# Performance work log

Measured on AMD Instinct MI355X. Metric: run time of the kernel, lower is better.

## Reference

```python
import jax, jax.numpy as jnp
import numpy as np

N_NODES = 50000
N_EDGES = 1600000
N_DECODE = 500000
D = 128
EPS = 1e-6


def _sage_conv(x, src, dst, Wl, bl, Wr, n_nodes):
    # PyG SAGEConv (mean aggr): out = lin_l(mean_{j in N(i)} x_j) + lin_r(x_i)
    msg = x[src]                                            # [E, D] gather
    s = jax.ops.segment_sum(msg, dst, num_segments=n_nodes) # [N, D]
    cnt = jax.ops.segment_sum(jnp.ones((src.shape[0],), x.dtype), dst,
                              num_segments=n_nodes)         # [N]
    aggr = s / jnp.maximum(cnt, 1.0)[:, None]
    return aggr @ Wl + bl + x @ Wr


def setup_inputs() -> dict:
    key = jax.random.key(0)
    ks = jax.random.split(key, 9)
    scale = 1.0 / np.sqrt(D)
    x = jax.random.normal(ks[0], (N_NODES, D), dtype=jnp.float32)
    edge_index = jax.random.randint(ks[1], (2, N_EDGES), 0, N_NODES, dtype=jnp.int64)
    decode_index = jax.random.randint(ks[2], (2, N_DECODE), 0, N_NODES, dtype=jnp.int64)
    W1l = jax.random.normal(ks[3], (D, D), dtype=jnp.float32) * scale
    b1 = jnp.zeros((D,), dtype=jnp.float32)
    W1r = jax.random.normal(ks[4], (D, D), dtype=jnp.float32) * scale
    W2l = jax.random.normal(ks[5], (D, D), dtype=jnp.float32) * scale
    b2 = jnp.zeros((D,), dtype=jnp.float32)
    W2r = jax.random.normal(ks[6], (D, D), dtype=jnp.float32) * scale
    return {"x": x, "edge_index": edge_index, "decode_index": decode_index,
            "W1l": W1l, "b1": b1, "W1r": W1r, "W2l": W2l, "b2": b2, "W2r": W2r}


def reference(x, edge_index, decode_index, W1l, b1, W1r, W2l, b2, W2r):
    src, dst = edge_index[0], edge_index[1]
    h = _sage_conv(x, src, dst, W1l, b1, W1r, N_NODES)
    h = jax.nn.relu(h)
    # dropout is a no-op in eval mode (training=False)
    h = _sage_conv(h, src, dst, W2l, b2, W2r, N_NODES)
    a = h[decode_index[0]]                                  # [Dk, D]
    b = h[decode_index[1]]
    num = jnp.sum(a * b, axis=1)
    denom = jnp.maximum(jnp.linalg.norm(a, axis=1) * jnp.linalg.norm(b, axis=1), EPS)
    return jax.nn.sigmoid(num / denom)
```

## Files before the change

### kernel.cpp

```cpp
#include <hip/hip_runtime.h>
#include <cstddef>

#define D 128
#define NBITS 7
#define BCAP2 6144
#define CHUNK 4096
#define BSTRIDE8 36

typedef float floatx4 __attribute__((ext_vector_type(4)));
typedef float floatx2 __attribute__((ext_vector_type(2)));

__device__ __forceinline__ int incl_scan64(int v) {
    const int lane = threadIdx.x & 63;
#pragma unroll
    for (int o = 1; o < 64; o <<= 1) {
        int u = __shfl_up(v, o);
        if (lane >= o) v += u;
    }
    return v;
}

__device__ __forceinline__ void accf8p(floatx2* a2, uint4 u) {
    unsigned w[4] = {u.x, u.y, u.z, u.w};
#pragma unroll
    for (int k = 0; k < 4; ++k) {
        a2[2 * k + 0] += __builtin_amdgcn_cvt_pk_f32_fp8((int)w[k], false);
        a2[2 * k + 1] += __builtin_amdgcn_cvt_pk_f32_fp8((int)w[k], true);
    }
}

__device__ __forceinline__ float dotf8(uint4 ua, uint4 ub) {
    unsigned wa[4] = {ua.x, ua.y, ua.z, ua.w};
    unsigned wb[4] = {ub.x, ub.y, ub.z, ub.w};
    float dot = 0.f;
#pragma unroll
    for (int k = 0; k < 4; ++k) {
        floatx2 alo = __builtin_amdgcn_cvt_pk_f32_fp8((int)wa[k], false);
        floatx2 ahi = __builtin_amdgcn_cvt_pk_f32_fp8((int)wa[k], true);
        floatx2 blo = __builtin_amdgcn_cvt_pk_f32_fp8((int)wb[k], false);
        floatx2 bhi = __builtin_amdgcn_cvt_pk_f32_fp8((int)wb[k], true);
        dot = fmaf(alo.x, blo.x, dot);
        dot = fmaf(alo.y, blo.y, dot);
        dot = fmaf(ahi.x, bhi.x, dot);
        dot = fmaf(ahi.y, bhi.y, dot);
    }
    return dot;
}

__global__ void __launch_bounds__(256) k1_prep_bucket(
        const float* __restrict__ x, unsigned* __restrict__ xf8,
        int nq, int nblk_a,
        const float* __restrict__ W1l, const float* __restrict__ W1r,
        const float* __restrict__ W2l, const float* __restrict__ W2r,
        unsigned* __restrict__ Wtf8,
        const int* __restrict__ src, const int* __restrict__ dst, int n_edges,
        unsigned* __restrict__ chunk_data, int* __restrict__ chunk_off,
        int nbuck) {
    int blk = (int)blockIdx.x;
    const int tid = threadIdx.x;
    if (blk < nblk_a) {
        int t = blk * 256 + tid;
        if (t < nq) {
            float4 v = ((const float4*)x)[t];
            int lo = __builtin_amdgcn_cvt_pk_fp8_f32(v.x, v.y, 0, false);
            xf8[t] = (unsigned)__builtin_amdgcn_cvt_pk_fp8_f32(v.z, v.w, lo, true);
        }
        return;
    }
    blk -= nblk_a;
    if (blk < 64) {
        int t2 = blk * 256 + tid;
        int widx = t2 >> 12;
        int within = t2 & 4095;
        int n = within >> 5;
        int g = within & 31;
        const float* W = (widx == 0) ? W1l : (widx == 1) ? W1r : (widx == 2) ? W2l : W2r;
        float w0 = W[(size_t)(4 * g + 0) * D + n];
        float w1 = W[(size_t)(4 * g + 1) * D + n];
        float w2 = W[(size_t)(4 * g + 2) * D + n];
        float w3 = W[(size_t)(4 * g + 3) * D + n];
        int lo = __builtin_amdgcn_cvt_pk_fp8_f32(w0, w1, 0, false);
        Wtf8[(size_t)widx * 4096 + (size_t)n * 32 + g] =
            (unsigned)__builtin_amdgcn_cvt_pk_fp8_f32(w2, w3, lo, true);
        return;
    }
    blk -= 64;
    __shared__ int cnt[512];
    __shared__ int cur[512];
    __shared__ int wsum[4];
    __shared__ unsigned ent[CHUNK];
    const int c = blk;
    const int e0 = c * CHUNK;
    const int n = min(CHUNK, n_edges - e0);
    cnt[tid] = 0;
    cnt[tid + 256] = 0;
    __syncthreads();
    for (int i = tid; i < n; i += 256)
        atomicAdd(&cnt[dst[e0 + i] >> NBITS], 1);
    __syncthreads();
    int c0 = cnt[2 * tid], c1 = cnt[2 * tid + 1];
    int v = c0 + c1;
    int s = incl_scan64(v);
    if ((tid & 63) == 63) wsum[tid >> 6] = s;
    __syncthreads();
    {
        int wv = tid >> 6;
        int add = (wv > 0 ? wsum[0] : 0) + (wv > 1 ? wsum[1] : 0) + (wv > 2 ? wsum[2] : 0);
        int excl = s + add - v;
        cur[2 * tid] = excl;
        cur[2 * tid + 1] = excl + c0;
        const int stride = nbuck + 1;
        if (2 * tid <= nbuck) chunk_off[(size_t)c * stride + 2 * tid] = excl;
        if (2 * tid + 1 <= nbuck) chunk_off[(size_t)c * stride + 2 * tid + 1] = excl + c0;
    }
    __syncthreads();
    for (int i = tid; i < n; i += 256) {
        int d = dst[e0 + i];
        int sv = src[e0 + i];
        int b = d >> NBITS;
        int p = atomicAdd(&cur[b], 1);
        ent[p] = ((unsigned)(d & ((1 << NBITS) - 1)) << 16) | (unsigned)sv;
    }
    __syncthreads();
    for (int i = tid; i < n; i += 256) chunk_data[(size_t)e0 + i] = ent[i];
}

__global__ void __launch_bounds__(512, 4) k2_layer1(
        const unsigned* __restrict__ chunk_data, const int* __restrict__ chunk_off,
        int nchunk, int nbuck,
        const unsigned* __restrict__ xf8, const unsigned* __restrict__ Wt,
        const float* __restrict__ bias,
        unsigned* __restrict__ csr16g, int* __restrict__ offsG,
        unsigned* __restrict__ aggf8, unsigned char* __restrict__ h1,
        int n_nodes) {
    __shared__ unsigned sB[2][128 * BSTRIDE8];
    __shared__ unsigned short lcsr[BCAP2];
    __shared__ int ndeg[128], ncur[128], offs_l[130];
    __shared__ int s_w0;
    const int tid = threadIdx.x;
    const int b = blockIdx.x;
    const int stride = nbuck + 1;

    if (tid < 128) ndeg[tid] = 0;
    __syncthreads();

    const int w = tid >> 1, half = tid & 1;
    for (int c = w; c < nchunk; c += 256) {
        int beg = chunk_off[(size_t)c * stride + b];
        int end = chunk_off[(size_t)c * stride + b + 1];
        const unsigned* cd = chunk_data + (size_t)c * CHUNK;
        for (int i = beg + half; i < end; i += 2)
            atomicAdd(&ndeg[cd[i] >> 16], 1);
    }
    __syncthreads();
    int v = 0, s = 0;
    if (tid < 128) {
        v = ndeg[tid];
        s = incl_scan64(v);
        if (tid == 63) s_w0 = s;
    }
    __syncthreads();
    if (tid < 128) {
        if (tid >= 64) s += s_w0;
        int excl = min(s - v, BCAP2);
        ncur[tid] = excl;
        offs_l[tid] = excl;
        offsG[(size_t)b * 129 + tid] = excl;
        if (tid == 127) {
            int tot = min(s, BCAP2);
            offs_l[128] = tot;
            offsG[(size_t)b * 129 + 128] = tot;
        }
    }
    __syncthreads();
    for (int c = w; c < nchunk; c += 256) {
        int beg = chunk_off[(size_t)c * stride + b];
        int end = chunk_off[(size_t)c * stride + b + 1];
        const unsigned* cd = chunk_data + (size_t)c * CHUNK;
        for (int i = beg + half; i < end; i += 2) {
            unsigned e = cd[i];
            int pos = atomicAdd(&ncur[e >> 16], 1);
            if (pos < BCAP2) lcsr[pos] = (unsigned short)(e & 0xffffu);
        }
    }
    for (int i = tid; i < 2048; i += 512) {
        int m = i >> 10;
        int col = (i >> 3) & 127;
        int c4 = (i & 7) * 4;
        *(uint4*)&sB[m][col * BSTRIDE8 + c4] =
            *(const uint4*)(Wt + (size_t)m * 4096 + (size_t)col * 32 + c4);
    }
    __syncthreads();
    {
        int tot = offs_l[128];
        int words = (tot + 1) >> 1;
        const unsigned* l32 = (const unsigned*)lcsr;
        for (int i = tid; i < words; i += 512)
            csr16g[(size_t)b * (BCAP2 / 2) + i] = l32[i];
    }
    const int wv2 = tid >> 6;
    const int lane = tid & 63;
    const int q = lane >> 3;
    const int l8 = lane & 7;
    const unsigned* fb = xf8 + (size_t)l8 * 4;
#pragma unroll
    for (int pass = 0; pass < 2; ++pass) {
        const int nl = pass * 64 + wv2 * 8 + q;
        const int beg = offs_l[nl];
        const int end = offs_l[nl + 1];
        floatx2 a2[8];
#pragma unroll
        for (int i = 0; i < 8; ++i) a2[i] = (floatx2)(0.f);
        int e = beg;
        for (; e + 2 <= end; e += 2) {
            int s0 = lcsr[e];
            int s1 = lcsr[e + 1];
            uint4 u0 = *(const uint4*)(fb + (size_t)s0 * 32);
            uint4 u1 = *(const uint4*)(fb + (size_t)s1 * 32);
            accf8p(a2, u0);
            accf8p(a2, u1);
        }
        if (e < end) {
            int s0 = lcsr[e];
            uint4 u0 = *(const uint4*)(fb + (size_t)s0 * 32);
            accf8p(a2, u0);
        }
        float r = 1.0f / fmaxf((float)(end - beg), 1.0f);
        unsigned o[4];
#pragma unroll
        for (int j = 0; j < 4; ++j) {
            int lo = __builtin_amdgcn_cvt_pk_fp8_f32(a2[2 * j].x * r, a2[2 * j].y * r, 0, false);
            o[j] = (unsigned)__builtin_amdgcn_cvt_pk_fp8_f32(a2[2 * j + 1].x * r,
                                                             a2[2 * j + 1].y * r, lo, true);
        }
        const int node = b * 128 + nl;
        if (node < n_nodes)
            *(uint4*)(aggf8 + (size_t)node * 32 + l8 * 4) = make_uint4(o[0], o[1], o[2], o[3]);
    }
    __syncthreads();

    const int li = lane & 15;
    const int quad = lane >> 4;
    const int node0 = b * 128 + wv2 * 16;
    if (node0 >= n_nodes) return;

    floatx4 acc[8];
#pragma unroll
    for (int t = 0; t < 8; ++t) acc[t] = (floatx4)(0.f);

    int arow = node0 + li;
    if (arow >= n_nodes) arow = n_nodes - 1;
    const unsigned* aptr1 = aggf8 + (size_t)arow * 32 + quad * 2;
    const unsigned* aptr2 = xf8 + (size_t)arow * 32 + quad * 2;
    const unsigned* sb0 = &sB[0][li * BSTRIDE8 + quad * 2];
    const unsigned* sb1 = &sB[1][li * BSTRIDE8 + quad * 2];

#pragma unroll
    for (int ks = 0; ks < 4; ++ks) {
        long af = *(const long*)(aptr1 + ks * 8);
#pragma unroll
        for (int ct = 0; ct < 8; ++ct) {
            long bf = *(const long*)(sb0 + ct * 16 * BSTRIDE8 + ks * 8);
            acc[ct] = __builtin_amdgcn_mfma_f32_16x16x32_fp8_fp8(af, bf, acc[ct], 0, 0, 0);
        }
    }
#pragma unroll
    for (int ks = 0; ks < 4; ++ks) {
        long af = *(const long*)(aptr2 + ks * 8);
#pragma unroll
        for (int ct = 0; ct < 8; ++ct) {
            long bf = *(const long*)(sb1 + ct * 16 * BSTRIDE8 + ks * 8);
            acc[ct] = __builtin_amdgcn_mfma_f32_16x16x32_fp8_fp8(af, bf, acc[ct], 0, 0, 0);
        }
    }
#pragma unroll
    for (int ct = 0; ct < 8; ++ct) {
        int col = ct * 16 + li;
        float bv = bias[col];
#pragma unroll
        for (int r = 0; r < 4; ++r) {
            int node = node0 + quad * 4 + r;
            float o = acc[ct][r] + bv;
            o = fmaxf(o, 0.f);
            int pk = __builtin_amdgcn_cvt_pk_fp8_f32(o, o, 0, false);
            if (node < n_nodes)
                h1[(size_t)node * D + col] = (unsigned char)(pk & 0xff);
        }
    }
}

__global__ void __launch_bounds__(512, 4) k3_layer2(
        const int* __restrict__ offsG, const unsigned* __restrict__ csr16g,
        const unsigned* __restrict__ h1f8, const unsigned* __restrict__ Wt2,
        const float* __restrict__ bias,
        unsigned* __restrict__ aggf8, unsigned char* __restrict__ h2,
        float* __restrict__ nrm2, int n_nodes) {
    __shared__ unsigned sB[2][128 * BSTRIDE8];
    __shared__ int offs_l[130];
    const int tid = threadIdx.x;
    const int b = blockIdx.x;
    if (tid < 129) offs_l[tid] = offsG[(size_t)b * 129 + tid];
    for (int i = tid; i < 2048; i += 512) {
        int m = i >> 10;
        int col = (i >> 3) & 127;
        int c4 = (i & 7) * 4;
        *(uint4*)&sB[m][col * BSTRIDE8 + c4] =
            *(const uint4*)(Wt2 + (size_t)m * 4096 + (size_t)col * 32 + c4);
    }
    __syncthreads();

    const unsigned short* csr = (const unsigned short*)csr16g + (size_t)b * BCAP2;
    const int wv2 = tid >> 6;
    const int lane = tid & 63;
    const int q = lane >> 3;
    const int l8 = lane & 7;
    const unsigned* fb = h1f8 + (size_t)l8 * 4;
#pragma unroll
    for (int pass = 0; pass < 2; ++pass) {
        const int nl = pass * 64 + wv2 * 8 + q;
        const int beg = offs_l[nl];
        const int end = offs_l[nl + 1];
        floatx2 a2[8];
#pragma unroll
        for (int i = 0; i < 8; ++i) a2[i] = (floatx2)(0.f);
        int e = beg;
        for (; e + 2 <= end; e += 2) {
            int s0 = csr[e];
            int s1 = csr[e + 1];
            uint4 u0 = *(const uint4*)(fb + (size_t)s0 * 32);
            uint4 u1 = *(const uint4*)(fb + (size_t)s1 * 32);
            accf8p(a2, u0);
            accf8p(a2, u1);
        }
        if (e < end) {
            int s0 = csr[e];
            uint4 u0 = *(const uint4*)(fb + (size_t)s0 * 32);
            accf8p(a2, u0);
        }
        float r = 1.0f / fmaxf((float)(end - beg), 1.0f);
        unsigned o[4];
#pragma unroll
        for (int j = 0; j < 4; ++j) {
            int lo = __builtin_amdgcn_cvt_pk_fp8_f32(a2[2 * j].x * r, a2[2 * j].y * r, 0, false);
            o[j] = (unsigned)__builtin_amdgcn_cvt_pk_fp8_f32(a2[2 * j + 1].x * r,
                                                             a2[2 * j + 1].y * r, lo, true);
        }
        const int node = b * 128 + nl;
        if (node < n_nodes)
            *(uint4*)(aggf8 + (size_t)node * 32 + l8 * 4) = make_uint4(o[0], o[1], o[2], o[3]);
    }
    __syncthreads();

    const int li = lane & 15;
    const int quad = lane >> 4;
    const int node0 = b * 128 + wv2 * 16;
    if (node0 >= n_nodes) return;

    floatx4 acc[8];
#pragma unroll
    for (int t = 0; t < 8; ++t) acc[t] = (floatx4)(0.f);

    int arow = node0 + li;
    if (arow >= n_nodes) arow = n_nodes - 1;
    const unsigned* aptr1 = aggf8 + (size_t)arow * 32 + quad * 2;
    const unsigned* aptr2 = h1f8 + (size_t)arow * 32 + quad * 2;
    const unsigned* sb0 = &sB[0][li * BSTRIDE8 + quad * 2];
    const unsigned* sb1 = &sB[1][li * BSTRIDE8 + quad * 2];

#pragma unroll
    for (int ks = 0; ks < 4; ++ks) {
        long af = *(const long*)(aptr1 + ks * 8);
#pragma unroll
        for (int ct = 0; ct < 8; ++ct) {
            long bf = *(const long*)(sb0 + ct * 16 * BSTRIDE8 + ks * 8);
            acc[ct] = __builtin_amdgcn_mfma_f32_16x16x32_fp8_fp8(af, bf, acc[ct], 0, 0, 0);
        }
    }
#pragma unroll
    for (int ks = 0; ks < 4; ++ks) {
        long af = *(const long*)(aptr2 + ks * 8);
#pragma unroll
        for (int ct = 0; ct < 8; ++ct) {
            long bf = *(const long*)(sb1 + ct * 16 * BSTRIDE8 + ks * 8);
            acc[ct] = __builtin_amdgcn_mfma_f32_16x16x32_fp8_fp8(af, bf, acc[ct], 0, 0, 0);
        }
    }
    float sq[4] = {0.f, 0.f, 0.f, 0.f};
#pragma unroll
    for (int ct = 0; ct < 8; ++ct) {
        int col = ct * 16 + li;
        float bv = bias[col];
#pragma unroll
        for (int r = 0; r < 4; ++r) {
            int node = node0 + quad * 4 + r;
            float o = acc[ct][r] + bv;
            int pk = __builtin_amdgcn_cvt_pk_fp8_f32(o, o, 0, false);
            floatx2 dq = __builtin_amdgcn_cvt_pk_f32_fp8(pk, false);
            sq[r] += dq.x * dq.x;
            if (node < n_nodes)
                h2[(size_t)node * D + col] = (unsigned char)(pk & 0xff);
        }
    }
#pragma unroll
    for (int r = 0; r < 4; ++r) {
        float sv = sq[r];
        sv += __shfl_xor(sv, 1);
        sv += __shfl_xor(sv, 2);
        sv += __shfl_xor(sv, 4);
        sv += __shfl_xor(sv, 8);
        int node = node0 + quad * 4 + r;
        if (li == 0 && node < n_nodes) nrm2[node] = sv;
    }
}

__global__ void decode_kernel(const unsigned* __restrict__ h8, const float* __restrict__ nrm2,
                              const int* __restrict__ ia, const int* __restrict__ ib,
                              float* __restrict__ out, int n_pairs) {
    int t = blockIdx.x * blockDim.x + threadIdx.x;
    int p = t >> 3;
    if (p >= n_pairs) return;
    int l8 = t & 7;
    int i0 = ia[p];
    int i1 = ib[p];
    uint4 ua = *(const uint4*)(h8 + (size_t)i0 * 32 + l8 * 4);
    uint4 ub = *(const uint4*)(h8 + (size_t)i1 * 32 + l8 * 4);
    float dot = dotf8(ua, ub);
    dot += __shfl_xor(dot, 1);
    dot += __shfl_xor(dot, 2);
    dot += __shfl_xor(dot, 4);
    if (l8 == 0) {
        float denom = fmaxf(sqrtf(nrm2[i0] * nrm2[i1]), 1e-6f);
        float s = dot / denom;
        out[p] = 1.0f / (1.0f + expf(-s));
    }
}


extern "C" void kernel_launch(void* const* d_in, const int* in_sizes, int n_in,
                              void* d_out, int out_size, void* d_ws, size_t ws_size,
                              hipStream_t stream) {
    const float* x   = (const float*)d_in[0];
    const int*   ei  = (const int*)d_in[1];
    const int*   di  = (const int*)d_in[2];
    const float* W1l = (const float*)d_in[3];
    const float* b1  = (const float*)d_in[4];
    const float* W1r = (const float*)d_in[5];
    const float* W2l = (const float*)d_in[6];
    const float* b2  = (const float*)d_in[7];
    const float* W2r = (const float*)d_in[8];

    const int N = in_sizes[0] / D;
    const int E = in_sizes[1] / 2;
    const int K = in_sizes[2] / 2;
    const size_t NQ = (size_t)N * (D / 4);
    const int NBUCK = (N + (1 << NBITS) - 1) >> NBITS;
    const int NCHUNK = (E + CHUNK - 1) / CHUNK;

    const int* src  = ei;
    const int* dstp = ei + E;
    const int* dia  = di;
    const int* dib  = di + K;

    unsigned* ws         = (unsigned*)d_ws;
    unsigned* chunk_data = ws;
    int*      chunk_off  = (int*)(chunk_data + E);
    unsigned* csr16g     = (unsigned*)(chunk_off + (size_t)NCHUNK * (NBUCK + 1));
    int*      offsG      = (int*)(csr16g + (size_t)NBUCK * (BCAP2 / 2));
    float*    nrm2       = (float*)(offsG + (size_t)NBUCK * 129);
    unsigned* Wtf8       = (unsigned*)(nrm2 + N);
    unsigned* xf8        = Wtf8 + 16384;
    unsigned* h1f8       = xf8 + NQ;
    unsigned* h2f8       = h1f8 + NQ;
    unsigned* aggf8      = h2f8 + NQ;

    float* out = (float*)d_out;

    const int nq = (int)NQ;
    const int nblk_a = (nq + 255) / 256;

    k1_prep_bucket<<<nblk_a + 64 + NCHUNK, 256, 0, stream>>>(
        x, xf8, nq, nblk_a, W1l, W1r, W2l, W2r, Wtf8,
        src, dstp, E, chunk_data, chunk_off, NBUCK);

    k2_layer1<<<NBUCK, 512, 0, stream>>>(
        chunk_data, chunk_off, NCHUNK, NBUCK, xf8, Wtf8, b1,
        csr16g, offsG, aggf8, (unsigned char*)h1f8, N);

    k3_layer2<<<NBUCK, 512, 0, stream>>>(
        offsG, csr16g, h1f8, Wtf8 + 8192, b2,
        aggf8, (unsigned char*)h2f8, nrm2, N);

    {
        long long threads = (long long)K * 8;
        int blocks = (int)((threads + 255) / 256);
        decode_kernel<<<blocks, 256, 0, stream>>>(h2f8, nrm2, dia, dib, out, K);
    }
}
```

Baseline: 232.9 us.

## Split CSR build from layer1, pad CSR rows, vectorize gathers, batch decode

CSR construction moves out of the fused layer-1 kernel into its own kernel. Both layer kernels now run at 64 nodes per block with 256 threads, which doubles the block count to fill the GPU better. Each node's CSR row is padded to a multiple of 8 so the gather can load 8 indices at once with a uint4 and issue 8 feature loads together for more memory-level parallelism. The decode kernel handles 8 pairs per thread group so more loads are in flight. In exchange there is one extra kernel launch, the global CSR is written and read back before layer 1, and padding eats into the per-bucket capacity.

```diff
diff --git a/kernel.cpp b/kernel.cpp
--- a/kernel.cpp
+++ b/kernel.cpp
@@ -6,6 +6,7 @@
 #define BCAP2 6144
 #define CHUNK 4096
 #define BSTRIDE8 36
+#define DNPP 8
 
 typedef float floatx4 __attribute__((ext_vector_type(4)));
 typedef float floatx2 __attribute__((ext_vector_type(2)));
@@ -109,9 +110,9 @@
         int excl = s + add - v;
         cur[2 * tid] = excl;
         cur[2 * tid + 1] = excl + c0;
-        const int stride = nbuck + 1;
-        if (2 * tid <= nbuck) chunk_off[(size_t)c * stride + 2 * tid] = excl;
-        if (2 * tid + 1 <= nbuck) chunk_off[(size_t)c * stride + 2 * tid + 1] = excl + c0;
+        const size_t base = (size_t)c * (nbuck + 1);
+        if (2 * tid <= nbuck) chunk_off[base + 2 * tid] = excl;
+        if (2 * tid + 1 <= nbuck) chunk_off[base + 2 * tid + 1] = excl + c0;
     }
     __syncthreads();
     for (int i = tid; i < n; i += 256) {
@@ -125,18 +126,14 @@
     for (int i = tid; i < n; i += 256) chunk_data[(size_t)e0 + i] = ent[i];
 }
 
-__global__ void __launch_bounds__(512, 4) k2_layer1(
+__global__ void __launch_bounds__(512) k2_csr(
         const unsigned* __restrict__ chunk_data, const int* __restrict__ chunk_off,
         int nchunk, int nbuck,
-        const unsigned* __restrict__ xf8, const unsigned* __restrict__ Wt,
-        const float* __restrict__ bias,
         unsigned* __restrict__ csr16g, int* __restrict__ offsG,
-        unsigned* __restrict__ aggf8, unsigned char* __restrict__ h1,
-        int n_nodes) {
-    __shared__ unsigned sB[2][128 * BSTRIDE8];
+        int* __restrict__ degG) {
     __shared__ unsigned short lcsr[BCAP2];
-    __shared__ int ndeg[128], ncur[128], offs_l[130];
-    __shared__ int s_w0;
+    __shared__ int ndeg[128], ncur[128];
+    __shared__ int s_w0, s_tot;
     const int tid = threadIdx.x;
     const int b = blockIdx.x;
     const int stride = nbuck + 1;
@@ -153,24 +150,23 @@
             atomicAdd(&ndeg[cd[i] >> 16], 1);
     }
     __syncthreads();
-    int v = 0, s = 0;
+    int v = 0, pd = 0, s = 0;
     if (tid < 128) {
         v = ndeg[tid];
-        s = incl_scan64(v);
+        pd = (v + 7) & ~7;
+        s = incl_scan64(pd);
         if (tid == 63) s_w0 = s;
     }
     __syncthreads();
     if (tid < 128) {
         if (tid >= 64) s += s_w0;
-        int excl = min(s - v, BCAP2);
+        int excl = min(s - pd, BCAP2);
+        int de = v;
+        if (excl + de > BCAP2) de = max(0, BCAP2 - excl);
         ncur[tid] = excl;
-        offs_l[tid] = excl;
-        offsG[(size_t)b * 129 + tid] = excl;
-        if (tid == 127) {
-            int tot = min(s, BCAP2);
-            offs_l[128] = tot;
-            offsG[(size_t)b * 129 + 128] = tot;
-        }
+        offsG[(size_t)b * 128 + tid] = excl;
+        degG[(size_t)b * 128 + tid] = de;
+        if (tid == 127) s_tot = min(s, BCAP2);
     }
     __syncthreads();
     for (int c = w; c < nchunk; c += 256) {
@@ -183,7 +179,91 @@
             if (pos < BCAP2) lcsr[pos] = (unsigned short)(e & 0xffffu);
         }
     }
-    for (int i = tid; i < 2048; i += 512) {
+    __syncthreads();
+    {
+        int tot = s_tot;
+        int words = (tot + 1) >> 1;
+        const unsigned* l32 = (const unsigned*)lcsr;
+        for (int i = tid; i < words; i += 512)
+            csr16g[(size_t)b * (BCAP2 / 2) + i] = l32[i];
+    }
+}
+
+__device__ __forceinline__ void gather64(
+        const unsigned short* __restrict__ csr,
+        const int* __restrict__ offs_l, const int* __restrict__ deg_l,
+        const unsigned* __restrict__ feat, unsigned* __restrict__ agg,
+        int bnode0, int n_nodes, int tid) {
+    const int wv = tid >> 6;
+    const int lane = tid & 63;
+    const int q = lane >> 3;
+    const int l8 = lane & 7;
+    const unsigned* fb = feat + (size_t)l8 * 4;
+#pragma unroll
+    for (int p2 = 0; p2 < 2; ++p2) {
+        const int nl = wv * 16 + p2 * 8 + q;
+        const int beg = offs_l[nl];
+        const int de = deg_l[nl];
+        const int end = beg + de;
+        floatx2 a2[8];
+#pragma unroll
+        for (int i = 0; i < 8; ++i) a2[i] = (floatx2)(0.f);
+        int e = beg;
+        for (; e + 8 <= end; e += 8) {
+            uint4 idv = *(const uint4*)(csr + e);
+            unsigned id0 = idv.x & 0xffffu, id1 = idv.x >> 16;
+            unsigned id2 = idv.y & 0xffffu, id3 = idv.y >> 16;
+            unsigned id4 = idv.z & 0xffffu, id5 = idv.z >> 16;
+            unsigned id6 = idv.w & 0xffffu, id7 = idv.w >> 16;
+            uint4 u0 = *(const uint4*)(fb + (size_t)id0 * 32);
+            uint4 u1 = *(const uint4*)(fb + (size_t)id1 * 32);
+            uint4 u2 = *(const uint4*)(fb + (size_t)id2 * 32);
+            uint4 u3 = *(const uint4*)(fb + (size_t)id3 * 32);
+            uint4 u4 = *(const uint4*)(fb + (size_t)id4 * 32);
+            uint4 u5 = *(const uint4*)(fb + (size_t)id5 * 32);
+            uint4 u6 = *(const uint4*)(fb + (size_t)id6 * 32);
+            uint4 u7 = *(const uint4*)(fb + (size_t)id7 * 32);
+            accf8p(a2, u0); accf8p(a2, u1); accf8p(a2, u2); accf8p(a2, u3);
+            accf8p(a2, u4); accf8p(a2, u5); accf8p(a2, u6); accf8p(a2, u7);
+        }
+        for (; e < end; ++e) {
+            uint4 u0 = *(const uint4*)(fb + (size_t)csr[e] * 32);
+            accf8p(a2, u0);
+        }
+        float r = 1.0f / fmaxf((float)de, 1.0f);
+        unsigned o[4];
+#pragma unroll
+        for (int j = 0; j < 4; ++j) {
+            int lo = __builtin_amdgcn_cvt_pk_fp8_f32(a2[2 * j].x * r, a2[2 * j].y * r, 0, false);
+            o[j] = (unsigned)__builtin_amdgcn_cvt_pk_fp8_f32(a2[2 * j + 1].x * r,
+                                                             a2[2 * j + 1].y * r, lo, true);
+        }
+        const int node = bnode0 + nl;
+        if (node < n_nodes)
+            *(uint4*)(agg + (size_t)node * 32 + l8 * 4) = make_uint4(o[0], o[1], o[2], o[3]);
+    }
+}
+
+__global__ void __launch_bounds__(256, 4) k3_layer1(
+        const int* __restrict__ offsG, const int* __restrict__ degG,
+        const unsigned* __restrict__ csr16g,
+        const unsigned* __restrict__ xf8, const unsigned* __restrict__ Wt,
+        const float* __restrict__ bias,
+        unsigned* __restrict__ aggf8, unsigned char* __restrict__ h1,
+        int n_nodes) {
+    __shared__ unsigned sB[2][128 * BSTRIDE8];
+    __shared__ int offs_l[64], deg_l[64];
+    const int tid = threadIdx.x;
+    const int b2 = blockIdx.x;
+    const int b = b2 >> 1;
+    const int hlf = b2 & 1;
+    const int bnode0 = b2 * 64;
+
+    if (tid < 64) {
+        offs_l[tid] = offsG[(size_t)b * 128 + hlf * 64 + tid];
+        deg_l[tid] = degG[(size_t)b * 128 + hlf * 64 + tid];
+    }
+    for (int i = tid; i < 2048; i += 256) {
         int m = i >> 10;
         int col = (i >> 3) & 127;
         int c4 = (i & 7) * 4;
@@ -191,57 +271,16 @@
             *(const uint4*)(Wt + (size_t)m * 4096 + (size_t)col * 32 + c4);
     }
     __syncthreads();
-    {
-        int tot = offs_l[128];
-        int words = (tot + 1) >> 1;
-        const unsigned* l32 = (const unsigned*)lcsr;
-        for (int i = tid; i < words; i += 512)
-            csr16g[(size_t)b * (BCAP2 / 2) + i] = l32[i];
-    }
-    const int wv2 = tid >> 6;
+
+    const unsigned short* csr = (const unsigned short*)csr16g + (size_t)b * BCAP2;
+    gather64(csr, offs_l, deg_l, xf8, aggf8, bnode0, n_nodes, tid);
+    __syncthreads();
+
     const int lane = tid & 63;
-    const int q = lane >> 3;
-    const int l8 = lane & 7;
-    const unsigned* fb = xf8 + (size_t)l8 * 4;
-#pragma unroll
-    for (int pass = 0; pass < 2; ++pass) {
-        const int nl = pass * 64 + wv2 * 8 + q;
-        const int beg = offs_l[nl];
-        const int end = offs_l[nl + 1];
-        floatx2 a2[8];
-#pragma unroll
-        for (int i = 0; i < 8; ++i) a2[i] = (floatx2)(0.f);
-        int e = beg;
-        for (; e + 2 <= end; e += 2) {
-            int s0 = lcsr[e];
-            int s1 = lcsr[e + 1];
-            uint4 u0 = *(const uint4*)(fb + (size_t)s0 * 32);
-            uint4 u1 = *(const uint4*)(fb + (size_t)s1 * 32);
-            accf8p(a2, u0);
-            accf8p(a2, u1);
-        }
-        if (e < end) {
-            int s0 = lcsr[e];
-            uint4 u0 = *(const uint4*)(fb + (size_t)s0 * 32);
-            accf8p(a2, u0);
-        }
-        float r = 1.0f / fmaxf((float)(end - beg), 1.0f);
-        unsigned o[4];
-#pragma unroll
-        for (int j = 0; j < 4; ++j) {
-            int lo = __builtin_amdgcn_cvt_pk_fp8_f32(a2[2 * j].x * r, a2[2 * j].y * r, 0, false);
-            o[j] = (unsigned)__builtin_amdgcn_cvt_pk_fp8_f32(a2[2 * j + 1].x * r,
-                                                             a2[2 * j + 1].y * r, lo, true);
-        }
-        const int node = b * 128 + nl;
-        if (node < n_nodes)
-            *(uint4*)(aggf8 + (size_t)node * 32 + l8 * 4) = make_uint4(o[0], o[1], o[2], o[3]);
-    }
-    __syncthreads();
-
+    const int wv = tid >> 6;
     const int li = lane & 15;
     const int quad = lane >> 4;
-    const int node0 = b * 128 + wv2 * 16;
+    const int node0 = bnode0 + wv * 16;
     if (node0 >= n_nodes) return;
 
     floatx4 acc[8];
@@ -250,14 +289,14 @@
 
     int arow = node0 + li;
     if (arow >= n_nodes) arow = n_nodes - 1;
-    const unsigned* aptr1 = aggf8 + (size_t)arow * 32 + quad * 2;
-    const unsigned* aptr2 = xf8 + (size_t)arow * 32 + quad * 2;
+    const unsigned* ap = aggf8 + (size_t)arow * 32 + quad * 2;
+    const unsigned* xp = xf8 + (size_t)arow * 32 + quad * 2;
     const unsigned* sb0 = &sB[0][li * BSTRIDE8 + quad * 2];
     const unsigned* sb1 = &sB[1][li * BSTRIDE8 + quad * 2];
 
 #pragma unroll
     for (int ks = 0; ks < 4; ++ks) {
-        long af = *(const long*)(aptr1 + ks * 8);
+        long af = *(const long*)(ap + ks * 8);
 #pragma unroll
         for (int ct = 0; ct < 8; ++ct) {
             long bf = *(const long*)(sb0 + ct * 16 * BSTRIDE8 + ks * 8);
@@ -266,7 +305,7 @@
     }
 #pragma unroll
     for (int ks = 0; ks < 4; ++ks) {
-        long af = *(const long*)(aptr2 + ks * 8);
+        long af = *(const long*)(xp + ks * 8);
 #pragma unroll
         for (int ct = 0; ct < 8; ++ct) {
             long bf = *(const long*)(sb1 + ct * 16 * BSTRIDE8 + ks * 8);
@@ -278,29 +317,37 @@
         int col = ct * 16 + li;
         float bv = bias[col];
 #pragma unroll
-        for (int r = 0; r < 4; ++r) {
-            int node = node0 + quad * 4 + r;
-            float o = acc[ct][r] + bv;
+        for (int r2 = 0; r2 < 4; ++r2) {
+            int node2 = node0 + quad * 4 + r2;
+            float o = acc[ct][r2] + bv;
             o = fmaxf(o, 0.f);
             int pk = __builtin_amdgcn_cvt_pk_fp8_f32(o, o, 0, false);
-            if (node < n_nodes)
-                h1[(size_t)node * D + col] = (unsigned char)(pk & 0xff);
-        }
-    }
-}
-
-__global__ void __launch_bounds__(512, 4) k3_layer2(
-        const int* __restrict__ offsG, const unsigned* __restrict__ csr16g,
+            if (node2 < n_nodes)
+                h1[(size_t)node2 * D + col] = (unsigned char)(pk & 0xff);
+        }
+    }
+}
+
+__global__ void __launch_bounds__(256, 4) k4_layer2(
+        const int* __restrict__ offsG, const int* __restrict__ degG,
+        const unsigned* __restrict__ csr16g,
         const unsigned* __restrict__ h1f8, const unsigned* __restrict__ Wt2,
         const float* __restrict__ bias,
         unsigned* __restrict__ aggf8, unsigned char* __restrict__ h2,
         float* __restrict__ nrm2, int n_nodes) {
     __shared__ unsigned sB[2][128 * BSTRIDE8];
-    __shared__ int offs_l[130];
+    __shared__ int offs_l[64], deg_l[64];
     const int tid = threadIdx.x;
-    const int b = blockIdx.x;
-    if (tid < 129) offs_l[tid] = offsG[(size_t)b * 129 + tid];
-    for (int i = tid; i < 2048; i += 512) {
+    const int b2 = blockIdx.x;
+    const int b = b2 >> 1;
+    const int hlf = b2 & 1;
+    const int bnode0 = b2 * 64;
+
+    if (tid < 64) {
+        offs_l[tid] = offsG[(size_t)b * 128 + hlf * 64 + tid];
+        deg_l[tid] = degG[(size_t)b * 128 + hlf * 64 + tid];
+    }
+    for (int i = tid; i < 2048; i += 256) {
         int m = i >> 10;
         int col = (i >> 3) & 127;
         int c4 = (i & 7) * 4;
@@ -310,50 +357,14 @@
     __syncthreads();
 
     const unsigned short* csr = (const unsigned short*)csr16g + (size_t)b * BCAP2;
-    const int wv2 = tid >> 6;
+    gather64(csr, offs_l, deg_l, h1f8, aggf8, bnode0, n_nodes, tid);
+    __syncthreads();
+
     const int lane = tid & 63;
-    const int q = lane >> 3;
-    const int l8 = lane & 7;
-    const unsigned* fb = h1f8 + (size_t)l8 * 4;
-#pragma unroll
-    for (int pass = 0; pass < 2; ++pass) {
-        const int nl = pass * 64 + wv2 * 8 + q;
-        const int beg = offs_l[nl];
-        const int end = offs_l[nl + 1];
-        floatx2 a2[8];
-#pragma unroll
-        for (int i = 0; i < 8; ++i) a2[i] = (floatx2)(0.f);
-        int e = beg;
-        for (; e + 2 <= end; e += 2) {
-            int s0 = csr[e];
-            int s1 = csr[e + 1];
-            uint4 u0 = *(const uint4*)(fb + (size_t)s0 * 32);
-            uint4 u1 = *(const uint4*)(fb + (size_t)s1 * 32);
-            accf8p(a2, u0);
-            accf8p(a2, u1);
-        }
-        if (e < end) {
-            int s0 = csr[e];
-            uint4 u0 = *(const uint4*)(fb + (size_t)s0 * 32);
-            accf8p(a2, u0);
-        }
-        float r = 1.0f / fmaxf((float)(end - beg), 1.0f);
-        unsigned o[4];
-#pragma unroll
-        for (int j = 0; j < 4; ++j) {
-            int lo = __builtin_amdgcn_cvt_pk_fp8_f32(a2[2 * j].x * r, a2[2 * j].y * r, 0, false);
-            o[j] = (unsigned)__builtin_amdgcn_cvt_pk_fp8_f32(a2[2 * j + 1].x * r,
-                                                             a2[2 * j + 1].y * r, lo, true);
-        }
-        const int node = b * 128 + nl;
-        if (node < n_nodes)
-            *(uint4*)(aggf8 + (size_t)node * 32 + l8 * 4) = make_uint4(o[0], o[1], o[2], o[3]);
-    }
-    __syncthreads();
-
+    const int wv = tid >> 6;
     const int li = lane & 15;
     const int quad = lane >> 4;
-    const int node0 = b * 128 + wv2 * 16;
+    const int node0 = bnode0 + wv * 16;
     if (node0 >= n_nodes) return;
 
     floatx4 acc[8];
@@ -362,14 +373,14 @@
 
     int arow = node0 + li;
     if (arow >= n_nodes) arow = n_nodes - 1;
-    const unsigned* aptr1 = aggf8 + (size_t)arow * 32 + quad * 2;
-    const unsigned* aptr2 = h1f8 + (size_t)arow * 32 + quad * 2;
+    const unsigned* ap = aggf8 + (size_t)arow * 32 + quad * 2;
+    const unsigned* xp = h1f8 + (size_t)arow * 32 + quad * 2;
     const unsigned* sb0 = &sB[0][li * BSTRIDE8 + quad * 2];
     const unsigned* sb1 = &sB[1][li * BSTRIDE8 + quad * 2];
 
 #pragma unroll
     for (int ks = 0; ks < 4; ++ks) {
-        long af = *(const long*)(aptr1 + ks * 8);
+        long af = *(const long*)(ap + ks * 8);
 #pragma unroll
         for (int ct = 0; ct < 8; ++ct) {
             long bf = *(const long*)(sb0 + ct * 16 * BSTRIDE8 + ks * 8);
@@ -378,7 +389,7 @@
     }
 #pragma unroll
     for (int ks = 0; ks < 4; ++ks) {
-        long af = *(const long*)(aptr2 + ks * 8);
+        long af = *(const long*)(xp + ks * 8);
 #pragma unroll
         for (int ct = 0; ct < 8; ++ct) {
             long bf = *(const long*)(sb1 + ct * 16 * BSTRIDE8 + ks * 8);
@@ -391,47 +402,62 @@
         int col = ct * 16 + li;
         float bv = bias[col];
 #pragma unroll
-        for (int r = 0; r < 4; ++r) {
-            int node = node0 + quad * 4 + r;
-            float o = acc[ct][r] + bv;
+        for (int r2 = 0; r2 < 4; ++r2) {
+            int node2 = node0 + quad * 4 + r2;
+            float o = acc[ct][r2] + bv;
             int pk = __builtin_amdgcn_cvt_pk_fp8_f32(o, o, 0, false);
             floatx2 dq = __builtin_amdgcn_cvt_pk_f32_fp8(pk, false);
-            sq[r] += dq.x * dq.x;
-            if (node < n_nodes)
-                h2[(size_t)node * D + col] = (unsigned char)(pk & 0xff);
-        }
-    }
-#pragma unroll
-    for (int r = 0; r < 4; ++r) {
-        float sv = sq[r];
+            sq[r2] += dq.x * dq.x;
+            if (node2 < n_nodes)
+                h2[(size_t)node2 * D + col] = (unsigned char)(pk & 0xff);
+        }
+    }
+#pragma unroll
+    for (int r2 = 0; r2 < 4; ++r2) {
+        float sv = sq[r2];
         sv += __shfl_xor(sv, 1);
         sv += __shfl_xor(sv, 2);
         sv += __shfl_xor(sv, 4);
         sv += __shfl_xor(sv, 8);
-        int node = node0 + quad * 4 + r;
-        if (li == 0 && node < n_nodes) nrm2[node] = sv;
-    }
-}
-
-__global__ void decode_kernel(const unsigned* __restrict__ h8, const float* __restrict__ nrm2,
-                              const int* __restrict__ ia, const int* __restrict__ ib,
-                              float* __restrict__ out, int n_pairs) {
-    int t = blockIdx.x * blockDim.x + threadIdx.x;
-    int p = t >> 3;
-    if (p >= n_pairs) return;
-    int l8 = t & 7;
-    int i0 = ia[p];
-    int i1 = ib[p];
-    uint4 ua = *(const uint4*)(h8 + (size_t)i0 * 32 + l8 * 4);
-    uint4 ub = *(const uint4*)(h8 + (size_t)i1 * 32 + l8 * 4);
-    float dot = dotf8(ua, ub);
-    dot += __shfl_xor(dot, 1);
-    dot += __shfl_xor(dot, 2);
-    dot += __shfl_xor(dot, 4);
-    if (l8 == 0) {
-        float denom = fmaxf(sqrtf(nrm2[i0] * nrm2[i1]), 1e-6f);
-        float s = dot / denom;
-        out[p] = 1.0f / (1.0f + expf(-s));
+        int node2 = node0 + quad * 4 + r2;
+        if (li == 0 && node2 < n_nodes) nrm2[node2] = sv;
+    }
+}
+
+__global__ void __launch_bounds__(256, 4) k5_decode(
+        const unsigned* __restrict__ h2, const float* __restrict__ nrm2,
+        const int* __restrict__ ia, const int* __restrict__ ib,
+        float* __restrict__ out, int n_pairs) {
+    const int tid = threadIdx.x;
+    const int l8 = tid & 7;
+    const int g = blockIdx.x * 32 + (tid >> 3);
+    const int strideP = gridDim.x * 32;
+    int pa[DNPP], pb[DNPP];
+#pragma unroll
+    for (int i = 0; i < DNPP; ++i) {
+        int p = g + i * strideP;
+        int pc = (p < n_pairs) ? p : 0;
+        pa[i] = ia[pc];
+        pb[i] = ib[pc];
+    }
+    uint4 ua[DNPP], ub[DNPP];
+#pragma unroll
+    for (int i = 0; i < DNPP; ++i) {
+        ua[i] = *(const uint4*)(h2 + (size_t)pa[i] * 32 + l8 * 4);
+        ub[i] = *(const uint4*)(h2 + (size_t)pb[i] * 32 + l8 * 4);
+    }
+#pragma unroll
+    for (int i = 0; i < DNPP; ++i) {
+        float dot = dotf8(ua[i], ub[i]);
+        dot += __shfl_xor(dot, 1);
+        dot += __shfl_xor(dot, 2);
+        dot += __shfl_xor(dot, 4);
+        int p = g + i * strideP;
+        if (l8 == 0 && p < n_pairs) {
+            float denom = fmaxf(sqrtf(nrm2[pa[i]] * nrm2[pb[i]]), 1e-6f);
+            float s = dot / denom;
+            out[p] = 1.0f / (1.0f + expf(-s));
+        }
     }
 }
 
@@ -452,7 +478,7 @@
     const int N = in_sizes[0] / D;
     const int E = in_sizes[1] / 2;
     const int K = in_sizes[2] / 2;
-    const size_t NQ = (size_t)N * (D / 4);
+    const size_t NQ = (size_t)N * 32;
     const int NBUCK = (N + (1 << NBITS) - 1) >> NBITS;
     const int NCHUNK = (E + CHUNK - 1) / CHUNK;
 
@@ -466,7 +492,8 @@
     int*      chunk_off  = (int*)(chunk_data + E);
     unsigned* csr16g     = (unsigned*)(chunk_off + (size_t)NCHUNK * (NBUCK + 1));
     int*      offsG      = (int*)(csr16g + (size_t)NBUCK * (BCAP2 / 2));
-    float*    nrm2       = (float*)(offsG + (size_t)NBUCK * 129);
+    int*      degG       = offsG + (size_t)NBUCK * 128;
+    float*    nrm2       = (float*)(degG + (size_t)NBUCK * 128);
     unsigned* Wtf8       = (unsigned*)(nrm2 + N);
     unsigned* xf8        = Wtf8 + 16384;
     unsigned* h1f8       = xf8 + NQ;
@@ -482,17 +509,18 @@
         x, xf8, nq, nblk_a, W1l, W1r, W2l, W2r, Wtf8,
         src, dstp, E, chunk_data, chunk_off, NBUCK);
 
-    k2_layer1<<<NBUCK, 512, 0, stream>>>(
-        chunk_data, chunk_off, NCHUNK, NBUCK, xf8, Wtf8, b1,
-        csr16g, offsG, aggf8, (unsigned char*)h1f8, N);
-
-    k3_layer2<<<NBUCK, 512, 0, stream>>>(
-        offsG, csr16g, h1f8, Wtf8 + 8192, b2,
-        aggf8, (unsigned char*)h2f8, nrm2, N);
+    k2_csr<<<NBUCK, 512, 0, stream>>>(
+        chunk_data, chunk_off, NCHUNK, NBUCK, csr16g, offsG, degG);
+
+    k3_layer1<<<NBUCK * 2, 256, 0, stream>>>(
+        offsG, degG, csr16g, xf8, Wtf8, b1, aggf8, (unsigned char*)h1f8, N);
+
+    k4_layer2<<<NBUCK * 2, 256, 0, stream>>>(
+        offsG, degG, csr16g, h1f8, Wtf8 + 8192, b2, aggf8,
+        (unsigned char*)h2f8, nrm2, N);
 
     {
-        long long threads = (long long)K * 8;
-        int blocks = (int)((threads + 255) / 256);
-        decode_kernel<<<blocks, 256, 0, stream>>>(h2f8, nrm2, dia, dib, out, K);
-    }
-}
+        int G = (K + 32 * DNPP - 1) / (32 * DNPP);
+        k5_decode<<<G, 256, 0, stream>>>(h2f8, nrm2, dia, dib, out, K);
+    }
+}
```

Measured after the change: 243.9 us. 1.05x slower.
